# Optimization experiments

Measured on AMD Instinct MI355X. Metric: run time of the kernel, lower is better.

The kernel has to match this reference:

```python
import jax, jax.numpy as jnp
import numpy as np

EPS = 1e-6
H, HKV, D = 24, 8, 128


def rms_norm(x, g):
    # x: [..., D], normalize over last dim
    var = jnp.mean(jnp.square(x), axis=-1, keepdims=True)
    return x * jax.lax.rsqrt(var + EPS) * g


def apply_rope(x, cache):
    # x: [B, S, h, D]; cache: [S, D] with cos in [:, :D/2], sin in [:, D/2:] (NEOX)
    half = x.shape[-1] // 2
    cos = cache[None, :, None, :half]
    sin = cache[None, :, None, half:]
    x1, x2 = x[..., :half], x[..., half:]
    return jnp.concatenate([x1 * cos - x2 * sin, x2 * cos + x1 * sin], axis=-1)


def make_cos_sin_cache(seq_len, head_dim):
    pos = np.arange(seq_len, dtype=np.float32)
    inv_freq = 1.0 / (10000.0 ** (np.arange(0, head_dim, 2, dtype=np.float32) / head_dim))
    ang = pos[:, None] * inv_freq[None, :]  # [S, D/2]
    return jnp.asarray(np.concatenate([np.cos(ang), np.sin(ang)], axis=-1))


def setup_inputs() -> dict:
    key = jax.random.key(0)
    ks = jax.random.split(key, 10)
    dim = H * D  # 3072
    kv_dim = HKV * D  # 1024
    s = 1.0 / np.sqrt(dim)
    return {
        "hidden_states": jax.random.normal(ks[0], (2, 2048, dim), jnp.float32),
        "encoder_hidden_states": jax.random.normal(ks[1], (2, 512, dim), jnp.float32),
        "Wq": jax.random.normal(ks[2], (dim, dim), jnp.float32) * s,
        "Wk": jax.random.normal(ks[3], (dim, kv_dim), jnp.float32) * s,
        "Wv": jax.random.normal(ks[4], (dim, kv_dim), jnp.float32) * s,
        "Wak": jax.random.normal(ks[5], (dim, kv_dim), jnp.float32) * s,
        "Wav": jax.random.normal(ks[6], (dim, kv_dim), jnp.float32) * s,
        "Wo": jax.random.normal(ks[7], (dim, dim), jnp.float32) * s,
        "gq": jnp.ones((D,), jnp.float32),
        "gk": jnp.ones((D,), jnp.float32),
        "gak": jnp.ones((D,), jnp.float32),
        "img_cache": make_cos_sin_cache(2048, D),
        "txt_cache": make_cos_sin_cache(512, D),
    }


def reference(hidden_states, encoder_hidden_states, Wq, Wk, Wv, Wak, Wav, Wo,
              gq, gk, gak, img_cache, txt_cache):
    B, Si, dim = hidden_states.shape
    St = encoder_hidden_states.shape[1]

    q = (hidden_states @ Wq).reshape(B, Si, H, D)
    k = (hidden_states @ Wk).reshape(B, Si, HKV, D)
    v = (hidden_states @ Wv).reshape(B, Si, HKV, D)
    tk = (encoder_hidden_states @ Wak).reshape(B, St, HKV, D)
    tv = (encoder_hidden_states @ Wav).reshape(B, St, HKV, D)

    q = rms_norm(q, gq)
    k = rms_norm(k, gk)
    tk = rms_norm(tk, gak)

    q = apply_rope(q, img_cache)
    k = apply_rope(k, img_cache)
    tk = apply_rope(tk, txt_cache)

    joint_k = jnp.concatenate([k, tk], axis=1)   # [B, Si+St, HKV, D]
    joint_v = jnp.concatenate([v, tv], axis=1)

    # GQA: expand kv heads to query heads
    rep = H // HKV
    joint_k = jnp.repeat(joint_k, rep, axis=2)   # [B, Skv, H, D]
    joint_v = jnp.repeat(joint_v, rep, axis=2)

    scale = 1.0 / np.sqrt(D)
    scores = jnp.einsum("bqhd,bkhd->bhqk", q, joint_k) * scale
    probs = jax.nn.softmax(scores, axis=-1)
    attn = jnp.einsum("bhqk,bkhd->bqhd", probs, joint_v)

    out = attn.reshape(B, Si, H * D) @ Wo
    return out
```

## Files before the change

### kernel.cpp

```cpp
#include <hip/hip_runtime.h>
#include <hip/hip_bf16.h>
#include <math.h>

typedef __bf16 bf16;
typedef __bf16 bf16x4 __attribute__((ext_vector_type(4)));
typedef __bf16 bf16x8 __attribute__((ext_vector_type(8)));
typedef float  f32x4  __attribute__((ext_vector_type(4)));

typedef __attribute__((address_space(1))) void gvoid_t;
typedef __attribute__((address_space(3))) void lvoid_t;

static __device__ __forceinline__ void gload16(const void* g, void* l) {
  __builtin_amdgcn_global_load_lds((gvoid_t*)g, (lvoid_t*)l, 16, 0, 0);
}

static __device__ __forceinline__ float fexp2(float x) {
  return __builtin_amdgcn_exp2f(x);
}

static __device__ __forceinline__ unsigned pack2bf(float lo, float hi) {
  unsigned short l = __builtin_bit_cast(unsigned short, (bf16)lo);
  unsigned short h = __builtin_bit_cast(unsigned short, (bf16)hi);
  return ((unsigned)h << 16) | (unsigned)l;
}

__global__ __launch_bounds__(256) void cvt_bf16(const float* __restrict__ in,
                                                bf16* __restrict__ out, int n8) {
  int i = blockIdx.x * 256 + threadIdx.x;
  if (i >= n8) return;
  const float4* p = (const float4*)(in + (size_t)i * 8);
  float4 v0 = p[0], v1 = p[1];
  bf16x8 o;
  o[0] = (bf16)v0.x; o[1] = (bf16)v0.y; o[2] = (bf16)v0.z; o[3] = (bf16)v0.w;
  o[4] = (bf16)v1.x; o[5] = (bf16)v1.y; o[6] = (bf16)v1.z; o[7] = (bf16)v1.w;
  *(bf16x8*)(out + (size_t)i * 8) = o;
}

__global__ __launch_bounds__(256) void tcvt(const float* __restrict__ W,
                                            bf16* __restrict__ Wt, int K, int N) {
  __shared__ float t[32][33];
  const int tid = threadIdx.x;
  const int r = tid >> 3, c4 = (tid & 7) * 4;
  const size_t grow = (size_t)(blockIdx.y * 32 + r);
  float4 v = *(const float4*)(W + grow * N + blockIdx.x * 32 + c4);
  t[r][c4 + 0] = v.x; t[r][c4 + 1] = v.y; t[r][c4 + 2] = v.z; t[r][c4 + 3] = v.w;
  __syncthreads();
  bf16x4 o = { (bf16)t[c4 + 0][r], (bf16)t[c4 + 1][r], (bf16)t[c4 + 2][r], (bf16)t[c4 + 3][r] };
  *(bf16x4*)(Wt + (size_t)(blockIdx.x * 32 + r) * K + blockIdx.y * 32 + c4) = o;
}

template <typename OutT>
__global__ __launch_bounds__(256) void gemm_bt(const bf16* __restrict__ A,
                                               const bf16* __restrict__ Bt,
                                               OutT* __restrict__ C,
                                               int N, int K) {
  __shared__ bf16 As[128 * 64];
  __shared__ bf16 Bs[128 * 64];
  const int tid = threadIdx.x;
  const int wid = tid >> 6, lane = tid & 63;
  const int g = lane >> 4, c = lane & 15;
  const int brow = blockIdx.y * 128, bcol = blockIdx.x * 128;
  const int wr = (wid >> 1) * 64, wc = (wid & 1) * 64;
  f32x4 acc[4][4] = {};

  for (int k0 = 0; k0 < K; k0 += 64) {
#pragma unroll
    for (int i = 0; i < 4; ++i) {
      const int off = i * 4096 + tid * 16;
      const int row = off >> 7, colb = off & 127;
      gload16((const char*)A + ((size_t)(brow + row) * K + k0) * 2 + colb,
              (char*)As + i * 4096 + wid * 1024);
      gload16((const char*)Bt + ((size_t)(bcol + row) * K + k0) * 2 + colb,
              (char*)Bs + i * 4096 + wid * 1024);
    }
    __syncthreads();
#pragma unroll
    for (int ks = 0; ks < 2; ++ks) {
      bf16x8 af[4], bfr[4];
#pragma unroll
      for (int t = 0; t < 4; ++t) {
        af[t]  = *(const bf16x8*)(As + (wr + t * 16 + c) * 64 + ks * 32 + g * 8);
        bfr[t] = *(const bf16x8*)(Bs + (wc + t * 16 + c) * 64 + ks * 32 + g * 8);
      }
#pragma unroll
      for (int mt = 0; mt < 4; ++mt)
#pragma unroll
        for (int nt = 0; nt < 4; ++nt)
          acc[mt][nt] = __builtin_amdgcn_mfma_f32_16x16x32_bf16(af[mt], bfr[nt], acc[mt][nt], 0, 0, 0);
    }
    __syncthreads();
  }
#pragma unroll
  for (int mt = 0; mt < 4; ++mt)
#pragma unroll
    for (int nt = 0; nt < 4; ++nt)
#pragma unroll
      for (int r = 0; r < 4; ++r) {
        const int row = brow + wr + mt * 16 + 4 * g + r;
        const int col = bcol + wc + nt * 16 + c;
        C[(size_t)row * N + col] = (OutT)acc[mt][nt][r];
      }
}

template <typename OutT>
__global__ __launch_bounds__(512, 2) void gemm8(const bf16* __restrict__ A,
                                                const bf16* __restrict__ Bt,
                                                OutT* __restrict__ C,
                                                int N, int K, int NBX) {
  __shared__ char As[4 * 8192];
  __shared__ char Bs[4 * 16384];
  const int tid = threadIdx.x;
  const int lane = tid & 63, wid = tid >> 6;
  const int g = lane >> 4, c = lane & 15;
  const int wm = wid >> 2, wn = wid & 3;
  const int cpx = gridDim.x >> 3;
  const int wgid = ((int)blockIdx.x & 7) * cpx + ((int)blockIdx.x >> 3);
  const int by = wgid / NBX, bx = wgid % NBX;
  const int brow = by * 128, bcol = bx * 256;
  const int KH = K >> 5;

  f32x4 acc[4][4] = {};

  int LA = wid * 1024 + lane * 16;
  int lnA = LA >> 7;
  int sA = ((LA >> 4) & 7) ^ (lnA & 7);
  const char* Abase = (const char*)(A + (size_t)(brow + lnA * 2 + (sA >> 2)) * K + (sA & 3) * 8);
  int LB0 = wid * 1024 + lane * 16;
  int ln0 = LB0 >> 7;
  int s0 = ((LB0 >> 4) & 7) ^ (ln0 & 7);
  const char* Bbase0 = (const char*)(Bt + (size_t)(bcol + ln0 * 2 + (s0 >> 2)) * K + (s0 & 3) * 8);
  int LB1 = 8192 + wid * 1024 + lane * 16;
  int ln1 = LB1 >> 7;
  int s1 = ((LB1 >> 4) & 7) ^ (ln1 & 7);
  const char* Bbase1 = (const char*)(Bt + (size_t)(bcol + ln1 * 2 + (s1 >> 2)) * K + (s1 & 3) * 8);

  auto stage = [&](int kh, int slot) {
    const size_t koff = (size_t)kh * 64;
    gload16(Abase + koff, As + slot * 8192 + wid * 1024);
    gload16(Bbase0 + koff, Bs + slot * 16384 + wid * 1024);
    gload16(Bbase1 + koff, Bs + slot * 16384 + 8192 + wid * 1024);
  };

  int offA[4], offB[4];
#pragma unroll
  for (int mf = 0; mf < 4; ++mf) {
    const int row = wm * 64 + mf * 16 + c;
    const int ln = row >> 1;
    const int s = (((row & 1) << 2) | g) ^ (ln & 7);
    offA[mf] = ln * 128 + s * 16;
  }
#pragma unroll
  for (int nf = 0; nf < 4; ++nf) {
    const int row = wn * 64 + nf * 16 + c;
    const int ln = row >> 1;
    const int s = (((row & 1) << 2) | g) ^ (ln & 7);
    offB[nf] = ln * 128 + s * 16;
  }

#define GEMM8_PHASE(PHI, KH3)                                                     \
  {                                                                               \
    bf16x8 af[4], bfr[4];                                                         \
    _Pragma("unroll") for (int mf = 0; mf < 4; ++mf)                              \
      af[mf] = *(const bf16x8*)(As + (PHI) * 8192 + offA[mf]);                    \
    _Pragma("unroll") for (int nf = 0; nf < 4; ++nf)                              \
      bfr[nf] = *(const bf16x8*)(Bs + (PHI) * 16384 + offB[nf]);                  \
    stage((KH3), ((PHI) + 3) & 3);                                                \
    asm volatile("s_waitcnt vmcnt(6)" ::: "memory");                              \
    __builtin_amdgcn_s_barrier();                                                 \
    asm volatile("s_waitcnt lgkmcnt(0)" ::: "memory");                            \
    __builtin_amdgcn_sched_barrier(0);                                            \
    __builtin_amdgcn_s_setprio(1);                                                \
    _Pragma("unroll") for (int mf = 0; mf < 4; ++mf)                              \
      _Pragma("unroll") for (int nf = 0; nf < 4; ++nf)                            \
        acc[mf][nf] = __builtin_amdgcn_mfma_f32_16x16x32_bf16(af[mf], bfr[nf],    \
                                                              acc[mf][nf], 0, 0, 0); \
    __builtin_amdgcn_s_setprio(0);                                                \
    __builtin_amdgcn_s_barrier();                                                 \
  }

  stage(0, 0); stage(1, 1); stage(2, 2);
  asm volatile("s_waitcnt vmcnt(6)" ::: "memory");
  __builtin_amdgcn_s_barrier();

  const int NIT = K >> 7;
  for (int it = 0; it < NIT; ++it) {
    const int kb = it * 4;
    const int kmax = KH - 1;
    GEMM8_PHASE(0, (kb + 3 < kmax ? kb + 3 : kmax));
    GEMM8_PHASE(1, (kb + 4 < kmax ? kb + 4 : kmax));
    GEMM8_PHASE(2, (kb + 5 < kmax ? kb + 5 : kmax));
    GEMM8_PHASE(3, (kb + 6 < kmax ? kb + 6 : kmax));
  }
#undef GEMM8_PHASE

  const int wr = wm * 64, wc = wn * 64;
#pragma unroll
  for (int mf = 0; mf < 4; ++mf)
#pragma unroll
    for (int nf = 0; nf < 4; ++nf)
#pragma unroll
      for (int r = 0; r < 4; ++r) {
        const int row = brow + wr + mf * 16 + 4 * g + r;
        const int col = bcol + wc + nf * 16 + c;
        C[(size_t)row * N + col] = (OutT)acc[mf][nf][r];
      }
}

__global__ __launch_bounds__(256) void nrope_q(bf16* __restrict__ q, int stride,
                                               const float* __restrict__ gw,
                                               const float* __restrict__ cache) {
  const float SC = 0.08838834764831845f * 1.4426950408889634f;
  const int w = blockIdx.x * 4 + (threadIdx.x >> 6);
  const int lane = threadIdx.x & 63;
  const int row = w / 24, head = w % 24;
  const int pos = row & 2047;
  bf16* p = q + (size_t)row * stride + head * 128;
  float x1 = (float)p[lane], x2 = (float)p[64 + lane];
  float ss = x1 * x1 + x2 * x2;
#pragma unroll
  for (int m = 32; m; m >>= 1) ss += __shfl_xor(ss, m);
  const float inv = rsqrtf(ss * (1.0f / 128.0f) + 1e-6f);
  const float xn1 = x1 * inv * gw[lane], xn2 = x2 * inv * gw[64 + lane];
  const float cs = cache[pos * 128 + lane] * SC, sn = cache[pos * 128 + 64 + lane] * SC;
  p[lane]      = (bf16)(xn1 * cs - xn2 * sn);
  p[64 + lane] = (bf16)(xn2 * cs + xn1 * sn);
}

__global__ __launch_bounds__(256) void nrope_k(const bf16* __restrict__ src, int stride, int base,
                                               bf16* __restrict__ kf,
                                               const float* __restrict__ gw,
                                               const float* __restrict__ cache,
                                               int S, int key_off) {
  const int w = blockIdx.x * 4 + (threadIdx.x >> 6);
  const int lane = threadIdx.x & 63;
  const int row = w >> 3, hkv = w & 7;
  const int b = row / S, s = row % S;
  const bf16* p = src + (size_t)row * stride + base + hkv * 128;
  float x1 = (float)p[lane], x2 = (float)p[64 + lane];
  float ss = x1 * x1 + x2 * x2;
#pragma unroll
  for (int m = 32; m; m >>= 1) ss += __shfl_xor(ss, m);
  const float inv = rsqrtf(ss * (1.0f / 128.0f) + 1e-6f);
  const float xn1 = x1 * inv * gw[lane], xn2 = x2 * inv * gw[64 + lane];
  const float cs = cache[s * 128 + lane], sn = cache[s * 128 + 64 + lane];
  bf16* o = kf + ((size_t)(b * 8 + hkv) * 2560 + key_off + s) * 128;
  const int dsw = lane ^ ((s & 7) << 3);
  o[dsw]      = (bf16)(xn1 * cs - xn2 * sn);
  o[64 + dsw] = (bf16)(xn2 * cs + xn1 * sn);
}

__global__ __launch_bounds__(256) void transpose_v(const bf16* __restrict__ src, int stride, int base,
                                                   bf16* __restrict__ vtp,
                                                   int S, int key_off) {
  __shared__ bf16 t[32][33];
  const int tid = threadIdx.x;
  const int bh = blockIdx.z;
  const int b = bh >> 3, hkv = bh & 7;
  const int s0 = blockIdx.x * 32, d0 = blockIdx.y * 32;
  const int r = tid >> 3, c4 = (tid & 7) * 4;
  bf16x4 v = *(const bf16x4*)(src + (size_t)(b * S + s0 + r) * stride + base + hkv * 128 + d0 + c4);
  t[r][c4 + 0] = v[0]; t[r][c4 + 1] = v[1]; t[r][c4 + 2] = v[2]; t[r][c4 + 3] = v[3];
  __syncthreads();
  bf16x4 o = { t[c4 + 0][r], t[c4 + 1][r], t[c4 + 2][r], t[c4 + 3][r] };
  *(bf16x4*)(vtp + ((size_t)bh * 128 + d0 + r) * 2560 + key_off + s0 + c4) = o;
}

__global__ __launch_bounds__(256, 2) void attn_kernel(const bf16* __restrict__ qf,
                                                      const bf16* __restrict__ kfsw,
                                                      const bf16* __restrict__ vtp,
                                                      bf16* __restrict__ attnb) {
  __shared__ bf16 Ks[2][64 * 128];
  __shared__ bf16 Vs[2][128 * 64];
  __shared__ char Ps[4][1280];
  const int tid = threadIdx.x;
  const int wid = tid >> 6, lane = tid & 63;
  const int g = lane >> 4, c = lane & 15;
  const int bid0 = blockIdx.x;
  const int bid  = (bid0 & 7) * 96 + (bid0 >> 3);
  const int qb = bid & 15;
  const int h  = (bid >> 4) % 24;
  const int b  = bid / 384;
  const int q0 = qb * 128 + wid * 32;
  const int hkv = h / 3;
  const char* kfB = (const char*)kfsw + (size_t)(b * 8 + hkv) * 2560 * 256;
  const char* vtB = (const char*)vtp  + (size_t)(b * 8 + hkv) * 128 * 5120;

  bf16x8 qfrag[2][4];
#pragma unroll
  for (int qt = 0; qt < 2; ++qt) {
    const size_t qrow = (size_t)(b * 2048 + q0 + qt * 16 + c) * 5120 + h * 128;
#pragma unroll
    for (int kc = 0; kc < 4; ++kc)
      qfrag[qt][kc] = *(const bf16x8*)(qf + qrow + kc * 32 + g * 8);
  }

  f32x4 ot[2][8] = {};
  float lsum[2] = { 0.f, 0.f };

  auto stage = [&](int key0, int buf) {
    {
      char* ldst = (char*)&Ks[buf][0] + wid * 4096;
      const char* gsrc = kfB + (size_t)(key0 + wid * 16) * 256
                       + (lane >> 4) * 256 + (lane & 15) * 16;
#pragma unroll
      for (int j = 0; j < 4; ++j)
        gload16(gsrc + j * 1024, ldst + j * 1024);
    }
    {
      char* ldst = (char*)&Vs[buf][0] + wid * 4096;
      const int r8 = lane >> 3, c8 = lane & 7;
      const char* gsrc = vtB + (size_t)(wid * 32 + r8) * 5120 + (size_t)key0 * 2
                       + ((c8 ^ r8) * 16);
#pragma unroll
      for (int j = 0; j < 4; ++j)
        gload16(gsrc + (size_t)j * 8 * 5120, ldst + j * 1024);
    }
  };

  stage(0, 0);
  __syncthreads();

  for (int it = 0; it < 40; ++it) {
    const int cur = it & 1;
    if (it + 1 < 40) stage((it + 1) * 64, cur ^ 1);

    const char* Kb = (const char*)&Ks[cur][0];
    const char* Vb = (const char*)&Vs[cur][0];

#pragma unroll
    for (int kb = 0; kb < 2; ++kb) {
      f32x4 s[2][2] = {};
      __builtin_amdgcn_s_setprio(1);
#pragma unroll
      for (int kc = 0; kc < 4; ++kc) {
        const int bsw = (kc * 64 + g * 16) ^ ((c & 7) << 4);
        bf16x8 a0 = *(const bf16x8*)(Kb + (kb * 32 + c) * 256 + bsw);
        bf16x8 a1 = *(const bf16x8*)(Kb + (kb * 32 + 16 + c) * 256 + bsw);
#pragma unroll
        for (int qt = 0; qt < 2; ++qt) {
          s[qt][0] = __builtin_amdgcn_mfma_f32_16x16x32_bf16(a0, qfrag[qt][kc], s[qt][0], 0, 0, 0);
          s[qt][1] = __builtin_amdgcn_mfma_f32_16x16x32_bf16(a1, qfrag[qt][kc], s[qt][1], 0, 0, 0);
        }
      }
      __builtin_amdgcn_s_setprio(0);

      bf16x8 vfrag[8];
#pragma unroll
      for (int dt = 0; dt < 8; ++dt)
        vfrag[dt] = *(const bf16x8*)(Vb + (dt * 16 + c) * 128 + (((kb * 4 + g) ^ (c & 7)) * 16));

#pragma unroll
      for (int qt = 0; qt < 2; ++qt) {
        float p0[4], p1[4];
#pragma unroll
        for (int r = 0; r < 4; ++r) {
          p0[r] = fexp2(s[qt][0][r]);
          p1[r] = fexp2(s[qt][1][r]);
          lsum[qt] += p0[r] + p1[r];
        }
        uint2 w0, w1;
        w0.x = pack2bf(p0[0], p0[1]); w0.y = pack2bf(p0[2], p0[3]);
        w1.x = pack2bf(p1[0], p1[1]); w1.y = pack2bf(p1[2], p1[3]);
        *(uint2*)(&Ps[wid][0] + c * 80 + 8 * g)      = w0;
        *(uint2*)(&Ps[wid][0] + c * 80 + 32 + 8 * g) = w1;
        bf16x8 pf = *(const bf16x8*)(&Ps[wid][0] + c * 80 + g * 16);
        __builtin_amdgcn_s_setprio(1);
#pragma unroll
        for (int dt = 0; dt < 8; ++dt)
          ot[qt][dt] = __builtin_amdgcn_mfma_f32_16x16x32_bf16(vfrag[dt], pf, ot[qt][dt], 0, 0, 0);
        __builtin_amdgcn_s_setprio(0);
      }
    }
    __syncthreads();
  }

  char* osm = (char*)&Ks[0][0] + wid * 8192;
#pragma unroll
  for (int qt = 0; qt < 2; ++qt) {
    float ls = lsum[qt];
    ls += __shfl_xor(ls, 16);
    ls += __shfl_xor(ls, 32);
    const float inv = 1.0f / ls;
    const int q = qt * 16 + c;
#pragma unroll
    for (int dt = 0; dt < 8; ++dt) {
      uint2 w2;
      w2.x = pack2bf(ot[qt][dt][0] * inv, ot[qt][dt][1] * inv);
      w2.y = pack2bf(ot[qt][dt][2] * inv, ot[qt][dt][3] * inv);
      *(uint2*)(osm + q * 256 + ((dt * 32 + 8 * g) ^ ((q & 7) << 4))) = w2;
    }
  }
  __syncthreads();
#pragma unroll
  for (int it = 0; it < 8; ++it) {
    const int off = it * 1024 + lane * 16;
    const int qrow = off >> 8, colb = off & 255;
    bf16x8 v = *(const bf16x8*)(osm + qrow * 256 + (colb ^ ((qrow & 7) << 4)));
    *(bf16x8*)((char*)attnb + ((size_t)(b * 2048 + q0 + qrow) * 3072 + h * 128) * 2 + colb) = v;
  }
}

extern "C" void kernel_launch(void* const* d_in, const int* in_sizes, int n_in,
                              void* d_out, int out_size, void* d_ws, size_t ws_size,
                              hipStream_t stream) {
  const float* hs     = (const float*)d_in[0];
  const float* ehs    = (const float*)d_in[1];
  const float* Wq     = (const float*)d_in[2];
  const float* Wk     = (const float*)d_in[3];
  const float* Wv     = (const float*)d_in[4];
  const float* Wak    = (const float*)d_in[5];
  const float* Wav    = (const float*)d_in[6];
  const float* Wo     = (const float*)d_in[7];
  const float* gq     = (const float*)d_in[8];
  const float* gk     = (const float*)d_in[9];
  const float* gak    = (const float*)d_in[10];
  const float* icache = (const float*)d_in[11];
  const float* tcache = (const float*)d_in[12];

  char* ws = (char*)d_ws;
  bf16* hsb    = (bf16*)(ws + 0);
  bf16* Wcomb  = (bf16*)(ws + 25165824);
  bf16* ehsb   = (bf16*)(ws + 56623104);
  bf16* Wacomb = (bf16*)(ws + 62914560);
  bf16* qkvC   = (bf16*)(ws + 75497472);
  bf16* tC     = (bf16*)(ws + 117440512);
  bf16* kf     = (bf16*)(ws + 121634816);
  bf16* Wot    = (bf16*)(ws + 25165824);
  bf16* vt     = (bf16*)(ws + 56623104);
  bf16* attnb  = hsb;

  cvt_bf16<<<6144, 256, 0, stream>>>(hs, hsb, 1572864);
  cvt_bf16<<<1536, 256, 0, stream>>>(ehs, ehsb, 393216);
  tcvt<<<dim3(96, 96), 256, 0, stream>>>(Wq,  Wcomb,                3072, 3072);
  tcvt<<<dim3(32, 96), 256, 0, stream>>>(Wk,  Wcomb + 3072 * 3072,  3072, 1024);
  tcvt<<<dim3(32, 96), 256, 0, stream>>>(Wv,  Wcomb + 4096 * 3072,  3072, 1024);
  tcvt<<<dim3(32, 96), 256, 0, stream>>>(Wak, Wacomb,               3072, 1024);
  tcvt<<<dim3(32, 96), 256, 0, stream>>>(Wav, Wacomb + 1024 * 3072, 3072, 1024);

  gemm8<bf16><<<640, 512, 0, stream>>>(hsb, Wcomb, qkvC, 5120, 3072, 20);
  gemm_bt<bf16><<<dim3(16, 8), 256, 0, stream>>>(ehsb, Wacomb, tC, 2048, 3072);

  tcvt<<<dim3(96, 96), 256, 0, stream>>>(Wo, Wot, 3072, 3072);

  nrope_q<<<24576, 256, 0, stream>>>(qkvC, 5120, gq, icache);
  nrope_k<<<8192, 256, 0, stream>>>(qkvC, 5120, 3072, kf, gk,  icache, 2048, 0);
  nrope_k<<<2048, 256, 0, stream>>>(tC,   2048, 0,    kf, gak, tcache, 512,  2048);
  transpose_v<<<dim3(64, 4, 16), 256, 0, stream>>>(qkvC, 5120, 4096, vt, 2048, 0);
  transpose_v<<<dim3(16, 4, 16), 256, 0, stream>>>(tC,   2048, 1024, vt, 512,  2048);

  attn_kernel<<<768, 256, 0, stream>>>(qkvC, kf, vt, attnb);

  gemm8<float><<<384, 512, 0, stream>>>(attnb, Wot, (float*)d_out, 3072, 3072, 12);
}
```

Measured before the change: 595.5 us.

## Enlarge GEMM block tile to 256x256 with XCD-aware block mapping

Replaces the 128x256 GEMM tile with a 256x256 tile, in which each wave computes a 128x64 output using 8x4 MFMA accumulators. The A staging buffer doubles, and each K-step issues four async global-to-LDS loads per thread. Block indices are remapped so each XCD owns two adjacent row tiles. This raises operand reuse and cuts global traffic, but halves the grid, increases register and LDS pressure, and may lower occupancy and CU utilisation.

```diff
diff --git a/kernel.cpp b/kernel.cpp
--- a/kernel.cpp
+++ b/kernel.cpp
@@ -103,48 +103,49 @@
 }
 
 template <typename OutT>
-__global__ __launch_bounds__(512, 2) void gemm8(const bf16* __restrict__ A,
-                                                const bf16* __restrict__ Bt,
-                                                OutT* __restrict__ C,
-                                                int N, int K, int NBX) {
-  __shared__ char As[4 * 8192];
+__global__ __launch_bounds__(512, 2) void gemm8w(const bf16* __restrict__ A,
+                                                 const bf16* __restrict__ Bt,
+                                                 OutT* __restrict__ C,
+                                                 int N, int K, int NBX) {
+  __shared__ char As[4 * 16384];
   __shared__ char Bs[4 * 16384];
   const int tid = threadIdx.x;
   const int lane = tid & 63, wid = tid >> 6;
   const int g = lane >> 4, c = lane & 15;
   const int wm = wid >> 2, wn = wid & 3;
-  const int cpx = gridDim.x >> 3;
-  const int wgid = ((int)blockIdx.x & 7) * cpx + ((int)blockIdx.x >> 3);
-  const int by = wgid / NBX, bx = wgid % NBX;
-  const int brow = by * 128, bcol = bx * 256;
+  const int xcd = (int)blockIdx.x & 7;
+  const int local = (int)blockIdx.x >> 3;
+  const int by = xcd * 2 + (local & 1);
+  const int bx = local >> 1;
+  const int brow = by * 256, bcol = bx * 256;
   const int KH = K >> 5;
 
-  f32x4 acc[4][4] = {};
-
-  int LA = wid * 1024 + lane * 16;
-  int lnA = LA >> 7;
-  int sA = ((LA >> 4) & 7) ^ (lnA & 7);
-  const char* Abase = (const char*)(A + (size_t)(brow + lnA * 2 + (sA >> 2)) * K + (sA & 3) * 8);
-  int LB0 = wid * 1024 + lane * 16;
-  int ln0 = LB0 >> 7;
-  int s0 = ((LB0 >> 4) & 7) ^ (ln0 & 7);
-  const char* Bbase0 = (const char*)(Bt + (size_t)(bcol + ln0 * 2 + (s0 >> 2)) * K + (s0 & 3) * 8);
-  int LB1 = 8192 + wid * 1024 + lane * 16;
-  int ln1 = LB1 >> 7;
-  int s1 = ((LB1 >> 4) & 7) ^ (ln1 & 7);
-  const char* Bbase1 = (const char*)(Bt + (size_t)(bcol + ln1 * 2 + (s1 >> 2)) * K + (s1 & 3) * 8);
+  f32x4 acc[8][4] = {};
+
+  const char* Ab[2];
+  const char* Bb[2];
+#pragma unroll
+  for (int cc = 0; cc < 2; ++cc) {
+    int L = cc * 8192 + tid * 16;
+    int ln = L >> 7;
+    int s = ((L >> 4) & 7) ^ (ln & 7);
+    int row = ln * 2 + (s >> 2), kg = s & 3;
+    Ab[cc] = (const char*)(A + (size_t)(brow + row) * K + kg * 8);
+    Bb[cc] = (const char*)(Bt + (size_t)(bcol + row) * K + kg * 8);
+  }
 
   auto stage = [&](int kh, int slot) {
     const size_t koff = (size_t)kh * 64;
-    gload16(Abase + koff, As + slot * 8192 + wid * 1024);
-    gload16(Bbase0 + koff, Bs + slot * 16384 + wid * 1024);
-    gload16(Bbase1 + koff, Bs + slot * 16384 + 8192 + wid * 1024);
+    gload16(Ab[0] + koff, As + slot * 16384 + wid * 1024);
+    gload16(Ab[1] + koff, As + slot * 16384 + 8192 + wid * 1024);
+    gload16(Bb[0] + koff, Bs + slot * 16384 + wid * 1024);
+    gload16(Bb[1] + koff, Bs + slot * 16384 + 8192 + wid * 1024);
   };
 
-  int offA[4], offB[4];
-#pragma unroll
-  for (int mf = 0; mf < 4; ++mf) {
-    const int row = wm * 64 + mf * 16 + c;
+  int offA[8], offB[4];
+#pragma unroll
+  for (int mf = 0; mf < 8; ++mf) {
+    const int row = wm * 128 + mf * 16 + c;
     const int ln = row >> 1;
     const int s = (((row & 1) << 2) | g) ^ (ln & 7);
     offA[mf] = ln * 128 + s * 16;
@@ -157,20 +158,20 @@
     offB[nf] = ln * 128 + s * 16;
   }
 
-#define GEMM8_PHASE(PHI, KH3)                                                     \
+#define GEMM8W_PHASE(PHI, KH3)                                                    \
   {                                                                               \
-    bf16x8 af[4], bfr[4];                                                         \
-    _Pragma("unroll") for (int mf = 0; mf < 4; ++mf)                              \
-      af[mf] = *(const bf16x8*)(As + (PHI) * 8192 + offA[mf]);                    \
+    bf16x8 af[8], bfr[4];                                                         \
+    _Pragma("unroll") for (int mf = 0; mf < 8; ++mf)                              \
+      af[mf] = *(const bf16x8*)(As + (PHI) * 16384 + offA[mf]);                   \
     _Pragma("unroll") for (int nf = 0; nf < 4; ++nf)                              \
       bfr[nf] = *(const bf16x8*)(Bs + (PHI) * 16384 + offB[nf]);                  \
     stage((KH3), ((PHI) + 3) & 3);                                                \
-    asm volatile("s_waitcnt vmcnt(6)" ::: "memory");                              \
+    asm volatile("s_waitcnt vmcnt(8)" ::: "memory");                              \
     __builtin_amdgcn_s_barrier();                                                 \
     asm volatile("s_waitcnt lgkmcnt(0)" ::: "memory");                            \
     __builtin_amdgcn_sched_barrier(0);                                            \
     __builtin_amdgcn_s_setprio(1);                                                \
-    _Pragma("unroll") for (int mf = 0; mf < 4; ++mf)                              \
+    _Pragma("unroll") for (int mf = 0; mf < 8; ++mf)                              \
       _Pragma("unroll") for (int nf = 0; nf < 4; ++nf)                            \
         acc[mf][nf] = __builtin_amdgcn_mfma_f32_16x16x32_bf16(af[mf], bfr[nf],    \
                                                               acc[mf][nf], 0, 0, 0); \
@@ -179,23 +180,23 @@
   }
 
   stage(0, 0); stage(1, 1); stage(2, 2);
-  asm volatile("s_waitcnt vmcnt(6)" ::: "memory");
+  asm volatile("s_waitcnt vmcnt(8)" ::: "memory");
   __builtin_amdgcn_s_barrier();
 
   const int NIT = K >> 7;
   for (int it = 0; it < NIT; ++it) {
     const int kb = it * 4;
     const int kmax = KH - 1;
-    GEMM8_PHASE(0, (kb + 3 < kmax ? kb + 3 : kmax));
-    GEMM8_PHASE(1, (kb + 4 < kmax ? kb + 4 : kmax));
-    GEMM8_PHASE(2, (kb + 5 < kmax ? kb + 5 : kmax));
-    GEMM8_PHASE(3, (kb + 6 < kmax ? kb + 6 : kmax));
-  }
-#undef GEMM8_PHASE
-
-  const int wr = wm * 64, wc = wn * 64;
-#pragma unroll
-  for (int mf = 0; mf < 4; ++mf)
+    GEMM8W_PHASE(0, (kb + 3 < kmax ? kb + 3 : kmax));
+    GEMM8W_PHASE(1, (kb + 4 < kmax ? kb + 4 : kmax));
+    GEMM8W_PHASE(2, (kb + 5 < kmax ? kb + 5 : kmax));
+    GEMM8W_PHASE(3, (kb + 6 < kmax ? kb + 6 : kmax));
+  }
+#undef GEMM8W_PHASE
+
+  const int wr = wm * 128, wc = wn * 64;
+#pragma unroll
+  for (int mf = 0; mf < 8; ++mf)
 #pragma unroll
     for (int nf = 0; nf < 4; ++nf)
 #pragma unroll
@@ -437,7 +438,7 @@
   tcvt<<<dim3(32, 96), 256, 0, stream>>>(Wak, Wacomb,               3072, 1024);
   tcvt<<<dim3(32, 96), 256, 0, stream>>>(Wav, Wacomb + 1024 * 3072, 3072, 1024);
 
-  gemm8<bf16><<<640, 512, 0, stream>>>(hsb, Wcomb, qkvC, 5120, 3072, 20);
+  gemm8w<bf16><<<320, 512, 0, stream>>>(hsb, Wcomb, qkvC, 5120, 3072, 20);
   gemm_bt<bf16><<<dim3(16, 8), 256, 0, stream>>>(ehsb, Wacomb, tC, 2048, 3072);
 
   tcvt<<<dim3(96, 96), 256, 0, stream>>>(Wo, Wot, 3072, 3072);
@@ -450,5 +451,5 @@
 
   attn_kernel<<<768, 256, 0, stream>>>(qkvC, kf, vt, attnb);
 
-  gemm8<float><<<384, 512, 0, stream>>>(attnb, Wot, (float*)d_out, 3072, 3072, 12);
-}
+  gemm8w<float><<<192, 512, 0, stream>>>(attnb, Wot, (float*)d_out, 3072, 3072, 12);
+}
```

After: 570.1 us. -4.3%, faster.
